# Optimization experiments

Measured on AMD Instinct MI355X. Metric: run time of the kernel, lower is better.

Reference implementation:

```python
import jax, jax.numpy as jnp
import numpy as np

# Geometry / discretization constants (mirrors WaveCell.__init__)
NX, NY = 192, 192
DT = 1e-3
CMAX = 1.0
H = DT * CMAX * np.sqrt(2.0) * 1.01  # auto-set h as in __init__ (satisfies CFL)
SRC_X, SRC_Y = 96, 32  # point source grid location


def _laplacian(y, inv_h2):
    # y: [B, Nx, Ny]; 5-point stencil with zero padding (conv2d padding=1)
    p = jnp.pad(y, ((0, 0), (1, 1), (1, 1)))
    return inv_h2 * (p[:, :-2, 1:-1] + p[:, 2:, 1:-1]
                     + p[:, 1:-1, :-2] + p[:, 1:-1, 2:] - 4.0 * y)


def setup_inputs() -> dict:
    key = jax.random.key(0)
    k1, k2, k3 = jax.random.split(key, 3)
    B, T = 4, 256
    x = jax.random.normal(k1, (B, T, 1), dtype=jnp.float32)
    # per-cell wave speed in [0,1) so cmax <= 1 (CFL-safe)
    c = jax.random.uniform(k2, (NX, NY), dtype=jnp.float32)
    # boundary absorber damping coefficient
    b = jax.random.uniform(k3, (NX, NY), dtype=jnp.float32)
    return {"x": x, "c": c, "b": b}


def reference(x, c, b):
    B, T = x.shape[0], x.shape[1]
    inv_h2 = 1.0 / (H * H)
    inv_dt2 = 1.0 / (DT * DT)
    a_inv = 1.0 / (inv_dt2 + 0.5 * b / DT)   # [Nx, Ny]
    coef2 = inv_dt2 - 0.5 * b / DT           # [Nx, Ny]
    c2 = c * c

    x_seq = jnp.transpose(x[..., 0], (1, 0))  # [T, B]

    def step(carry, xt):
        y1, y2 = carry  # fields one and two steps ago
        y = a_inv * (2.0 * inv_dt2 * y1 - coef2 * y2 + c2 * _laplacian(y1, inv_h2))
        y = y.at[:, SRC_X, SRC_Y].add(xt)  # point source injection
        return (y, y1), y

    y0 = jnp.zeros((B, NX, NY), dtype=x.dtype)
    _, ys = jax.lax.scan(step, (y0, y0), x_seq)  # ys: [T, B, Nx, Ny]
    return jnp.transpose(ys, (1, 0, 2, 3))       # [B, T, Nx, Ny]
```

## Files before the change

kernel.cpp:

```cpp
#include <hip/hip_runtime.h>


#define NXg 192
#define NYg 192
#define BATCH 4
#define TSTEPS 256
#define CELLS (NXg * NYg)

#define TS 24
#define KSTEP 16
#define EXT 56
#define LROWS (EXT + 2)
#define LPITCH 68
#define LSZ (LROWS * LPITCH)
#define NTHREADS 448

#define SRC_X 96
#define SRC_Y 32

__global__ __launch_bounds__(NTHREADS) void wave_tile_kernel(
    const float* __restrict__ cgp, const float* __restrict__ bgp,
    const float* __restrict__ x, float* __restrict__ out, int t0) {
  __shared__ float buf0[LSZ];
  __shared__ float buf1[LSZ];

  const int tid = threadIdx.x;
  const int lr = tid >> 3;
  const int lg = tid & 7;
  const int bcol = blockIdx.x;
  const int brow = blockIdx.y;
  const int bb = blockIdx.z;
  const int r0 = brow * TS - KSTEP;
  const int c0 = bcol * TS - KSTEP;
  const int obase = bb * TSTEPS * CELLS;
  const float inv_h2 = (float)(1.0 / (2.0 * 1.01 * 1.01 * 1.0e-3 * 1.0e-3));

  const int gr = r0 + lr;
  const int gc = c0 + 8 * lg;
  const bool id = (lg < 7) && (gr >= 0) && (gr < NXg) && (gc >= 0) && (gc < NYg);
  const bool til = (lr >= KSTEP) && (lr < KSTEP + TS) && (lg >= 2) && (lg < 5);
  const bool hs = (SRC_X >= r0) && (SRC_X < r0 + EXT) &&
                  (SRC_Y >= c0) && (SRC_Y < c0 + EXT);
  const int gofs = id ? (gr * NYg + gc) : 0;

  const float4 z4 = make_float4(0.f, 0.f, 0.f, 0.f);

  float4 cv0 = z4, cv1 = z4, bv0 = z4, bv1 = z4;
  float4 yc0 = z4, yc1 = z4, yp0 = z4, yp1 = z4;
  if (id) {
    cv0 = *(const float4*)(cgp + gofs);
    cv1 = *(const float4*)(cgp + gofs + 4);
    bv0 = *(const float4*)(bgp + gofs);
    bv1 = *(const float4*)(bgp + gofs + 4);
    if (t0 > 0) {
      yc0 = *(const float4*)(out + obase + (t0 - 1) * CELLS + gofs);
      yc1 = *(const float4*)(out + obase + (t0 - 1) * CELLS + gofs + 4);
      yp0 = *(const float4*)(out + obase + (t0 - 2) * CELLS + gofs);
      yp1 = *(const float4*)(out + obase + (t0 - 2) * CELLS + gofs + 4);
    }
  }
  float xs[KSTEP];
  {
    const float4* xp = (const float4*)(x + bb * TSTEPS + t0);
    float4 a0 = xp[0], a1 = xp[1], a2 = xp[2], a3 = xp[3];
    xs[0] = a0.x; xs[1] = a0.y; xs[2] = a0.z; xs[3] = a0.w;
    xs[4] = a1.x; xs[5] = a1.y; xs[6] = a1.z; xs[7] = a1.w;
    xs[8] = a2.x; xs[9] = a2.y; xs[10] = a2.z; xs[11] = a2.w;
    xs[12] = a3.x; xs[13] = a3.y; xs[14] = a3.z; xs[15] = a3.w;
  }

  float4 Dc0 = z4, Dc1 = z4, Ey0 = z4, Ey1 = z4, G0 = z4, G1 = z4;
  float4 sm0 = z4, sm1 = z4;
  if (id) {
    float ai;
    ai = 1.0f / (1.0e6f + 500.0f * bv0.x);
    Dc0.x = 2.0e6f * ai; Ey0.x = (1.0e6f - 500.0f * bv0.x) * ai;
    G0.x = (cv0.x * cv0.x) * inv_h2 * ai;
    ai = 1.0f / (1.0e6f + 500.0f * bv0.y);
    Dc0.y = 2.0e6f * ai; Ey0.y = (1.0e6f - 500.0f * bv0.y) * ai;
    G0.y = (cv0.y * cv0.y) * inv_h2 * ai;
    ai = 1.0f / (1.0e6f + 500.0f * bv0.z);
    Dc0.z = 2.0e6f * ai; Ey0.z = (1.0e6f - 500.0f * bv0.z) * ai;
    G0.z = (cv0.z * cv0.z) * inv_h2 * ai;
    ai = 1.0f / (1.0e6f + 500.0f * bv0.w);
    Dc0.w = 2.0e6f * ai; Ey0.w = (1.0e6f - 500.0f * bv0.w) * ai;
    G0.w = (cv0.w * cv0.w) * inv_h2 * ai;
    ai = 1.0f / (1.0e6f + 500.0f * bv1.x);
    Dc1.x = 2.0e6f * ai; Ey1.x = (1.0e6f - 500.0f * bv1.x) * ai;
    G1.x = (cv1.x * cv1.x) * inv_h2 * ai;
    ai = 1.0f / (1.0e6f + 500.0f * bv1.y);
    Dc1.y = 2.0e6f * ai; Ey1.y = (1.0e6f - 500.0f * bv1.y) * ai;
    G1.y = (cv1.y * cv1.y) * inv_h2 * ai;
    ai = 1.0f / (1.0e6f + 500.0f * bv1.z);
    Dc1.z = 2.0e6f * ai; Ey1.z = (1.0e6f - 500.0f * bv1.z) * ai;
    G1.z = (cv1.z * cv1.z) * inv_h2 * ai;
    ai = 1.0f / (1.0e6f + 500.0f * bv1.w);
    Dc1.w = 2.0e6f * ai; Ey1.w = (1.0e6f - 500.0f * bv1.w) * ai;
    G1.w = (cv1.w * cv1.w) * inv_h2 * ai;
    if (gr == SRC_X) {
      sm0.x = (gc + 0 == SRC_Y) ? 1.0f : 0.0f;
      sm0.y = (gc + 1 == SRC_Y) ? 1.0f : 0.0f;
      sm0.z = (gc + 2 == SRC_Y) ? 1.0f : 0.0f;
      sm0.w = (gc + 3 == SRC_Y) ? 1.0f : 0.0f;
      sm1.x = (gc + 4 == SRC_Y) ? 1.0f : 0.0f;
      sm1.y = (gc + 5 == SRC_Y) ? 1.0f : 0.0f;
      sm1.z = (gc + 6 == SRC_Y) ? 1.0f : 0.0f;
      sm1.w = (gc + 7 == SRC_Y) ? 1.0f : 0.0f;
    }
  }

  const int lo = (lr + 1) * LPITCH + 4 + 8 * lg;
  *(float4*)&buf0[lo] = yc0;
  *(float4*)&buf0[lo + 4] = yc1;
  __syncthreads();

  float* ping = buf0;
  float* pong = buf1;

  float4 pv0 = z4, pv1 = z4;
  float* pop = out;

#define CELL(dst, up_, dn_, lf_, rt_, D_, E_, Gc_, y_, p_)              \
  {                                                                     \
    float s_ = fmaf(-4.0f, y_, (up_ + dn_) + (lf_ + rt_));              \
    dst = fmaf(Gc_, s_, fmaf(-E_, p_, D_ * y_));                        \
  }

#pragma unroll
  for (int j = 0; j < KSTEP; ++j) {
    const float xt = xs[j];
    float* op = out + obase + (t0 + j) * CELLS;

    if (j > 0 && til) {
      *(float4*)(pop + gofs) = pv0;
      *(float4*)(pop + gofs + 4) = pv1;
    }

    const bool alive = (lr >= j + 1) && (lr <= 54 - j);
    if (alive) {
      float lqw = __shfl_up(yc1.w, 1);
      lqw = (lg == 0) ? 0.0f : lqw;
      float rqx = __shfl_down(yc0.x, 1);
      rqx = (lg == 7) ? 0.0f : rqx;

      float4 up0 = *(float4*)&ping[lo - LPITCH];
      float4 up1 = *(float4*)&ping[lo - LPITCH + 4];
      float4 dn0 = *(float4*)&ping[lo + LPITCH];
      float4 dn1 = *(float4*)&ping[lo + LPITCH + 4];

      float4 val0, val1;
      CELL(val0.x, up0.x, dn0.x, lqw,    yc0.y, Dc0.x, Ey0.x, G0.x, yc0.x, yp0.x);
      CELL(val0.y, up0.y, dn0.y, yc0.x,  yc0.z, Dc0.y, Ey0.y, G0.y, yc0.y, yp0.y);
      CELL(val0.z, up0.z, dn0.z, yc0.y,  yc0.w, Dc0.z, Ey0.z, G0.z, yc0.z, yp0.z);
      CELL(val0.w, up0.w, dn0.w, yc0.z,  yc1.x, Dc0.w, Ey0.w, G0.w, yc0.w, yp0.w);
      CELL(val1.x, up1.x, dn1.x, yc0.w,  yc1.y, Dc1.x, Ey1.x, G1.x, yc1.x, yp1.x);
      CELL(val1.y, up1.y, dn1.y, yc1.x,  yc1.z, Dc1.y, Ey1.y, G1.y, yc1.y, yp1.y);
      CELL(val1.z, up1.z, dn1.z, yc1.y,  yc1.w, Dc1.z, Ey1.z, G1.z, yc1.z, yp1.z);
      CELL(val1.w, up1.w, dn1.w, yc1.z,  rqx,   Dc1.w, Ey1.w, G1.w, yc1.w, yp1.w);

      if (hs) {
        val0.x = fmaf(sm0.x, xt, val0.x);
        val0.y = fmaf(sm0.y, xt, val0.y);
        val0.z = fmaf(sm0.z, xt, val0.z);
        val0.w = fmaf(sm0.w, xt, val0.w);
        val1.x = fmaf(sm1.x, xt, val1.x);
        val1.y = fmaf(sm1.y, xt, val1.y);
        val1.z = fmaf(sm1.z, xt, val1.z);
        val1.w = fmaf(sm1.w, xt, val1.w);
      }

      yp0 = yc0; yp1 = yc1;
      yc0 = val0; yc1 = val1;

      if (j < KSTEP - 1) {
        *(float4*)&pong[lo] = val0;
        *(float4*)&pong[lo + 4] = val1;
      }

      pv0 = val0; pv1 = val1;
    }
    pop = op;

    if (j < KSTEP - 1) {
      asm volatile("s_waitcnt lgkmcnt(0)\n\ts_barrier" ::: "memory");
    }
    float* tmp = ping; ping = pong; pong = tmp;
  }
#undef CELL

  if (til) {
    *(float4*)(pop + gofs) = pv0;
    *(float4*)(pop + gofs + 4) = pv1;
  }
}

extern "C" void kernel_launch(void* const* d_in, const int* in_sizes, int n_in,
                              void* d_out, int out_size, void* d_ws,
                              size_t ws_size, hipStream_t stream) {
  const float* x = (const float*)d_in[0];
  const float* c = (const float*)d_in[1];
  const float* b = (const float*)d_in[2];
  float* out = (float*)d_out;

  dim3 grid(NXg / TS, NYg / TS, BATCH);
  for (int t0 = 0; t0 < TSTEPS; t0 += KSTEP) {
    wave_tile_kernel<<<grid, NTHREADS, 0, stream>>>(c, b, x, out, t0);
  }
}
```

Baseline: 317.9 us.

## Replace per-chunk kernel launches with one cooperative persistent kernel using grid sync

The host loop of 16 kernel launches is replaced by a single cooperative launch. Each block loops over the time chunks and calls a grid-wide sync between them. The per-block coefficients (damping and wave-speed terms) are computed once instead of once per launch. This removes launch gaps and the repeated coefficient setup, in exchange for grid barrier cost, with a fallback to multi-launch if the cooperative launch fails.

```diff
diff --git a/kernel.cpp b/kernel.cpp
--- a/kernel.cpp
+++ b/kernel.cpp
@@ -1,4 +1,7 @@
 #include <hip/hip_runtime.h>
+#include <hip/hip_cooperative_groups.h>
+
+namespace cg = cooperative_groups;
 
 
 #define NXg 192
@@ -18,11 +21,13 @@
 #define SRC_X 96
 #define SRC_Y 32
 
-__global__ __launch_bounds__(NTHREADS) void wave_tile_kernel(
+__global__ __launch_bounds__(NTHREADS) void wave_kernel(
     const float* __restrict__ cgp, const float* __restrict__ bgp,
-    const float* __restrict__ x, float* __restrict__ out, int t0) {
+    const float* __restrict__ x, float* __restrict__ out,
+    int t0b, int t0e) {
   __shared__ float buf0[LSZ];
   __shared__ float buf1[LSZ];
+  cg::grid_group grid = cg::this_grid();
 
   const int tid = threadIdx.x;
   const int lr = tid >> 3;
@@ -45,33 +50,13 @@
 
   const float4 z4 = make_float4(0.f, 0.f, 0.f, 0.f);
 
-  float4 cv0 = z4, cv1 = z4, bv0 = z4, bv1 = z4;
-  float4 yc0 = z4, yc1 = z4, yp0 = z4, yp1 = z4;
-  if (id) {
-    cv0 = *(const float4*)(cgp + gofs);
-    cv1 = *(const float4*)(cgp + gofs + 4);
-    bv0 = *(const float4*)(bgp + gofs);
-    bv1 = *(const float4*)(bgp + gofs + 4);
-    if (t0 > 0) {
-      yc0 = *(const float4*)(out + obase + (t0 - 1) * CELLS + gofs);
-      yc1 = *(const float4*)(out + obase + (t0 - 1) * CELLS + gofs + 4);
-      yp0 = *(const float4*)(out + obase + (t0 - 2) * CELLS + gofs);
-      yp1 = *(const float4*)(out + obase + (t0 - 2) * CELLS + gofs + 4);
-    }
-  }
-  float xs[KSTEP];
-  {
-    const float4* xp = (const float4*)(x + bb * TSTEPS + t0);
-    float4 a0 = xp[0], a1 = xp[1], a2 = xp[2], a3 = xp[3];
-    xs[0] = a0.x; xs[1] = a0.y; xs[2] = a0.z; xs[3] = a0.w;
-    xs[4] = a1.x; xs[5] = a1.y; xs[6] = a1.z; xs[7] = a1.w;
-    xs[8] = a2.x; xs[9] = a2.y; xs[10] = a2.z; xs[11] = a2.w;
-    xs[12] = a3.x; xs[13] = a3.y; xs[14] = a3.z; xs[15] = a3.w;
-  }
-
   float4 Dc0 = z4, Dc1 = z4, Ey0 = z4, Ey1 = z4, G0 = z4, G1 = z4;
   float4 sm0 = z4, sm1 = z4;
   if (id) {
+    float4 cv0 = *(const float4*)(cgp + gofs);
+    float4 cv1 = *(const float4*)(cgp + gofs + 4);
+    float4 bv0 = *(const float4*)(bgp + gofs);
+    float4 bv1 = *(const float4*)(bgp + gofs + 4);
     float ai;
     ai = 1.0f / (1.0e6f + 500.0f * bv0.x);
     Dc0.x = 2.0e6f * ai; Ey0.x = (1.0e6f - 500.0f * bv0.x) * ai;
@@ -110,15 +95,6 @@
   }
 
   const int lo = (lr + 1) * LPITCH + 4 + 8 * lg;
-  *(float4*)&buf0[lo] = yc0;
-  *(float4*)&buf0[lo + 4] = yc1;
-  __syncthreads();
-
-  float* ping = buf0;
-  float* pong = buf1;
-
-  float4 pv0 = z4, pv1 = z4;
-  float* pop = out;
 
 #define CELL(dst, up_, dn_, lf_, rt_, D_, E_, Gc_, y_, p_)              \
   {                                                                     \
@@ -126,72 +102,105 @@
     dst = fmaf(Gc_, s_, fmaf(-E_, p_, D_ * y_));                        \
   }
 
+  for (int t0 = t0b; t0 < t0e; t0 += KSTEP) {
+    if (t0 > t0b) {
+      grid.sync();
+    }
+
+    float4 yc0 = z4, yc1 = z4, yp0 = z4, yp1 = z4;
+    if (id && t0 > 0) {
+      yc0 = *(const float4*)(out + obase + (t0 - 1) * CELLS + gofs);
+      yc1 = *(const float4*)(out + obase + (t0 - 1) * CELLS + gofs + 4);
+      yp0 = *(const float4*)(out + obase + (t0 - 2) * CELLS + gofs);
+      yp1 = *(const float4*)(out + obase + (t0 - 2) * CELLS + gofs + 4);
+    }
+    float xs[KSTEP];
+    {
+      const float4* xp = (const float4*)(x + bb * TSTEPS + t0);
+      float4 a0 = xp[0], a1 = xp[1], a2 = xp[2], a3 = xp[3];
+      xs[0] = a0.x; xs[1] = a0.y; xs[2] = a0.z; xs[3] = a0.w;
+      xs[4] = a1.x; xs[5] = a1.y; xs[6] = a1.z; xs[7] = a1.w;
+      xs[8] = a2.x; xs[9] = a2.y; xs[10] = a2.z; xs[11] = a2.w;
+      xs[12] = a3.x; xs[13] = a3.y; xs[14] = a3.z; xs[15] = a3.w;
+    }
+
+    *(float4*)&buf0[lo] = yc0;
+    *(float4*)&buf0[lo + 4] = yc1;
+    asm volatile("s_waitcnt lgkmcnt(0)\n\ts_barrier" ::: "memory");
+
+    float* ping = buf0;
+    float* pong = buf1;
+
+    float4 pv0 = z4, pv1 = z4;
+    float* pop = out;
+
 #pragma unroll
-  for (int j = 0; j < KSTEP; ++j) {
-    const float xt = xs[j];
-    float* op = out + obase + (t0 + j) * CELLS;
-
-    if (j > 0 && til) {
+    for (int j = 0; j < KSTEP; ++j) {
+      const float xt = xs[j];
+      float* op = out + obase + (t0 + j) * CELLS;
+
+      if (j > 0 && til) {
+        *(float4*)(pop + gofs) = pv0;
+        *(float4*)(pop + gofs + 4) = pv1;
+      }
+
+      const bool alive = (lr >= j + 1) && (lr <= 54 - j);
+      if (alive) {
+        float lqw = __shfl_up(yc1.w, 1);
+        lqw = (lg == 0) ? 0.0f : lqw;
+        float rqx = __shfl_down(yc0.x, 1);
+        rqx = (lg == 7) ? 0.0f : rqx;
+
+        float4 up0 = *(float4*)&ping[lo - LPITCH];
+        float4 up1 = *(float4*)&ping[lo - LPITCH + 4];
+        float4 dn0 = *(float4*)&ping[lo + LPITCH];
+        float4 dn1 = *(float4*)&ping[lo + LPITCH + 4];
+
+        float4 val0, val1;
+        CELL(val0.x, up0.x, dn0.x, lqw,    yc0.y, Dc0.x, Ey0.x, G0.x, yc0.x, yp0.x);
+        CELL(val0.y, up0.y, dn0.y, yc0.x,  yc0.z, Dc0.y, Ey0.y, G0.y, yc0.y, yp0.y);
+        CELL(val0.z, up0.z, dn0.z, yc0.y,  yc0.w, Dc0.z, Ey0.z, G0.z, yc0.z, yp0.z);
+        CELL(val0.w, up0.w, dn0.w, yc0.z,  yc1.x, Dc0.w, Ey0.w, G0.w, yc0.w, yp0.w);
+        CELL(val1.x, up1.x, dn1.x, yc0.w,  yc1.y, Dc1.x, Ey1.x, G1.x, yc1.x, yp1.x);
+        CELL(val1.y, up1.y, dn1.y, yc1.x,  yc1.z, Dc1.y, Ey1.y, G1.y, yc1.y, yp1.y);
+        CELL(val1.z, up1.z, dn1.z, yc1.y,  yc1.w, Dc1.z, Ey1.z, G1.z, yc1.z, yp1.z);
+        CELL(val1.w, up1.w, dn1.w, yc1.z,  rqx,   Dc1.w, Ey1.w, G1.w, yc1.w, yp1.w);
+
+        if (hs) {
+          val0.x = fmaf(sm0.x, xt, val0.x);
+          val0.y = fmaf(sm0.y, xt, val0.y);
+          val0.z = fmaf(sm0.z, xt, val0.z);
+          val0.w = fmaf(sm0.w, xt, val0.w);
+          val1.x = fmaf(sm1.x, xt, val1.x);
+          val1.y = fmaf(sm1.y, xt, val1.y);
+          val1.z = fmaf(sm1.z, xt, val1.z);
+          val1.w = fmaf(sm1.w, xt, val1.w);
+        }
+
+        yp0 = yc0; yp1 = yc1;
+        yc0 = val0; yc1 = val1;
+
+        if (j < KSTEP - 1) {
+          *(float4*)&pong[lo] = val0;
+          *(float4*)&pong[lo + 4] = val1;
+        }
+
+        pv0 = val0; pv1 = val1;
+      }
+      pop = op;
+
+      if (j < KSTEP - 1) {
+        asm volatile("s_waitcnt lgkmcnt(0)\n\ts_barrier" ::: "memory");
+      }
+      float* tmp = ping; ping = pong; pong = tmp;
+    }
+
+    if (til) {
       *(float4*)(pop + gofs) = pv0;
       *(float4*)(pop + gofs + 4) = pv1;
     }
-
-    const bool alive = (lr >= j + 1) && (lr <= 54 - j);
-    if (alive) {
-      float lqw = __shfl_up(yc1.w, 1);
-      lqw = (lg == 0) ? 0.0f : lqw;
-      float rqx = __shfl_down(yc0.x, 1);
-      rqx = (lg == 7) ? 0.0f : rqx;
-
-      float4 up0 = *(float4*)&ping[lo - LPITCH];
-      float4 up1 = *(float4*)&ping[lo - LPITCH + 4];
-      float4 dn0 = *(float4*)&ping[lo + LPITCH];
-      float4 dn1 = *(float4*)&ping[lo + LPITCH + 4];
-
-      float4 val0, val1;
-      CELL(val0.x, up0.x, dn0.x, lqw,    yc0.y, Dc0.x, Ey0.x, G0.x, yc0.x, yp0.x);
-      CELL(val0.y, up0.y, dn0.y, yc0.x,  yc0.z, Dc0.y, Ey0.y, G0.y, yc0.y, yp0.y);
-      CELL(val0.z, up0.z, dn0.z, yc0.y,  yc0.w, Dc0.z, Ey0.z, G0.z, yc0.z, yp0.z);
-      CELL(val0.w, up0.w, dn0.w, yc0.z,  yc1.x, Dc0.w, Ey0.w, G0.w, yc0.w, yp0.w);
-      CELL(val1.x, up1.x, dn1.x, yc0.w,  yc1.y, Dc1.x, Ey1.x, G1.x, yc1.x, yp1.x);
-      CELL(val1.y, up1.y, dn1.y, yc1.x,  yc1.z, Dc1.y, Ey1.y, G1.y, yc1.y, yp1.y);
-      CELL(val1.z, up1.z, dn1.z, yc1.y,  yc1.w, Dc1.z, Ey1.z, G1.z, yc1.z, yp1.z);
-      CELL(val1.w, up1.w, dn1.w, yc1.z,  rqx,   Dc1.w, Ey1.w, G1.w, yc1.w, yp1.w);
-
-      if (hs) {
-        val0.x = fmaf(sm0.x, xt, val0.x);
-        val0.y = fmaf(sm0.y, xt, val0.y);
-        val0.z = fmaf(sm0.z, xt, val0.z);
-        val0.w = fmaf(sm0.w, xt, val0.w);
-        val1.x = fmaf(sm1.x, xt, val1.x);
-        val1.y = fmaf(sm1.y, xt, val1.y);
-        val1.z = fmaf(sm1.z, xt, val1.z);
-        val1.w = fmaf(sm1.w, xt, val1.w);
-      }
-
-      yp0 = yc0; yp1 = yc1;
-      yc0 = val0; yc1 = val1;
-
-      if (j < KSTEP - 1) {
-        *(float4*)&pong[lo] = val0;
-        *(float4*)&pong[lo + 4] = val1;
-      }
-
-      pv0 = val0; pv1 = val1;
-    }
-    pop = op;
-
-    if (j < KSTEP - 1) {
-      asm volatile("s_waitcnt lgkmcnt(0)\n\ts_barrier" ::: "memory");
-    }
-    float* tmp = ping; ping = pong; pong = tmp;
   }
 #undef CELL
-
-  if (til) {
-    *(float4*)(pop + gofs) = pv0;
-    *(float4*)(pop + gofs + 4) = pv1;
-  }
 }
 
 extern "C" void kernel_launch(void* const* d_in, const int* in_sizes, int n_in,
@@ -203,7 +212,15 @@
   float* out = (float*)d_out;
 
   dim3 grid(NXg / TS, NYg / TS, BATCH);
-  for (int t0 = 0; t0 < TSTEPS; t0 += KSTEP) {
-    wave_tile_kernel<<<grid, NTHREADS, 0, stream>>>(c, b, x, out, t0);
+  int t0b = 0, t0e = TSTEPS;
+  const float* ca = c; const float* ba = b; const float* xa = x; float* oa = out;
+  void* args[] = {(void*)&ca, (void*)&ba, (void*)&xa, (void*)&oa,
+                  (void*)&t0b, (void*)&t0e};
+  hipError_t err = hipLaunchCooperativeKernel(
+      (const void*)wave_kernel, grid, dim3(NTHREADS), args, 0, stream);
+  if (err != hipSuccess) {
+    for (int t0 = 0; t0 < TSTEPS; t0 += KSTEP) {
+      wave_kernel<<<grid, NTHREADS, 0, stream>>>(c, b, x, out, t0, t0 + KSTEP);
+    }
   }
 }
```

New measurement: 774.9 us. +143.7%, slower.

## Advance two time steps per barrier using redundant neighbor-row computation

Applied to the files above, without the earlier changes.

Each thread now also computes the rows directly above and below its own at step t, keeping their previous values and coefficients in registers. With those it can produce its row at step t+1 without an LDS round trip, so the number of LDS exchanges and barriers per 16-step launch is halved. The cost is about three times the stencil arithmetic per step, more registers for the extra coefficients and history, and extra zeroed halo rows in shared memory.

```diff
diff --git a/kernel.cpp b/kernel.cpp
--- a/kernel.cpp
+++ b/kernel.cpp
@@ -10,7 +10,7 @@
 #define TS 24
 #define KSTEP 16
 #define EXT 56
-#define LROWS (EXT + 2)
+#define LROWS 60
 #define LPITCH 68
 #define LSZ (LROWS * LPITCH)
 #define NTHREADS 448
@@ -18,7 +18,42 @@
 #define SRC_X 96
 #define SRC_Y 32
 
-__global__ __launch_bounds__(NTHREADS) void wave_tile_kernel(
+__device__ __forceinline__ void mkcoef(float4 cv, float4 bv, float inv_h2,
+                                       float4& D, float4& E, float4& Gq) {
+  float ai;
+  ai = 1.0f / (1.0e6f + 500.0f * bv.x);
+  D.x = 2.0e6f * ai; E.x = (1.0e6f - 500.0f * bv.x) * ai; Gq.x = cv.x * cv.x * inv_h2 * ai;
+  ai = 1.0f / (1.0e6f + 500.0f * bv.y);
+  D.y = 2.0e6f * ai; E.y = (1.0e6f - 500.0f * bv.y) * ai; Gq.y = cv.y * cv.y * inv_h2 * ai;
+  ai = 1.0f / (1.0e6f + 500.0f * bv.z);
+  D.z = 2.0e6f * ai; E.z = (1.0e6f - 500.0f * bv.z) * ai; Gq.z = cv.z * cv.z * inv_h2 * ai;
+  ai = 1.0f / (1.0e6f + 500.0f * bv.w);
+  D.w = 2.0e6f * ai; E.w = (1.0e6f - 500.0f * bv.w) * ai; Gq.w = cv.w * cv.w * inv_h2 * ai;
+}
+
+#define CELL(dst, up_, dn_, lf_, rt_, D_, E_, G_, y_, p_)             \
+  {                                                                   \
+    float s_ = fmaf(-4.0f, y_, (up_ + dn_) + (lf_ + rt_));            \
+    dst = fmaf(G_, s_, fmaf(-E_, p_, D_ * y_));                       \
+  }
+
+#define ROW8(vA, vB, uA, uB, dA, dB, cA, cB, lq, rq, Da, Db, Ea, Eb, Ga, Gb, pA, pB) \
+  CELL(vA.x, uA.x, dA.x, lq,   cA.y, Da.x, Ea.x, Ga.x, cA.x, pA.x);   \
+  CELL(vA.y, uA.y, dA.y, cA.x, cA.z, Da.y, Ea.y, Ga.y, cA.y, pA.y);   \
+  CELL(vA.z, uA.z, dA.z, cA.y, cA.w, Da.z, Ea.z, Ga.z, cA.z, pA.z);   \
+  CELL(vA.w, uA.w, dA.w, cA.z, cB.x, Da.w, Ea.w, Ga.w, cA.w, pA.w);   \
+  CELL(vB.x, uB.x, dB.x, cA.w, cB.y, Db.x, Eb.x, Gb.x, cB.x, pB.x);   \
+  CELL(vB.y, uB.y, dB.y, cB.x, cB.z, Db.y, Eb.y, Gb.y, cB.y, pB.y);   \
+  CELL(vB.z, uB.z, dB.z, cB.y, cB.w, Db.z, Eb.z, Gb.z, cB.z, pB.z);   \
+  CELL(vB.w, uB.w, dB.w, cB.z, rq,   Db.w, Eb.w, Gb.w, cB.w, pB.w);
+
+#define ADDSRC(vA, vB, sA, sB, xt_)                                   \
+  vA.x = fmaf(sA.x, xt_, vA.x); vA.y = fmaf(sA.y, xt_, vA.y);         \
+  vA.z = fmaf(sA.z, xt_, vA.z); vA.w = fmaf(sA.w, xt_, vA.w);         \
+  vB.x = fmaf(sB.x, xt_, vB.x); vB.y = fmaf(sB.y, xt_, vB.y);         \
+  vB.z = fmaf(sB.z, xt_, vB.z); vB.w = fmaf(sB.w, xt_, vB.w);
+
+__global__ __launch_bounds__(NTHREADS) void wave_kernel(
     const float* __restrict__ cgp, const float* __restrict__ bgp,
     const float* __restrict__ x, float* __restrict__ out, int t0) {
   __shared__ float buf0[LSZ];
@@ -37,26 +72,75 @@
 
   const int gr = r0 + lr;
   const int gc = c0 + 8 * lg;
-  const bool id = (lg < 7) && (gr >= 0) && (gr < NXg) && (gc >= 0) && (gc < NYg);
+  const bool colOK = (lg < 7) && (gc >= 0) && (gc < NYg);
+  const bool idC = colOK && (gr >= 0) && (gr < NXg);
+  const bool idU = colOK && (gr - 1 >= 0) && (gr - 1 < NXg);
+  const bool idD = colOK && (gr + 1 >= 0) && (gr + 1 < NXg);
   const bool til = (lr >= KSTEP) && (lr < KSTEP + TS) && (lg >= 2) && (lg < 5);
-  const bool hs = (SRC_X >= r0) && (SRC_X < r0 + EXT) &&
+  const bool hs = (SRC_X >= r0 - 1) && (SRC_X <= r0 + EXT) &&
                   (SRC_Y >= c0) && (SRC_Y < c0 + EXT);
-  const int gofs = id ? (gr * NYg + gc) : 0;
+  const int ofsC = idC ? (gr * NYg + gc) : 0;
+  const int ofsU = idU ? ((gr - 1) * NYg + gc) : 0;
+  const int ofsD = idD ? ((gr + 1) * NYg + gc) : 0;
 
   const float4 z4 = make_float4(0.f, 0.f, 0.f, 0.f);
 
-  float4 cv0 = z4, cv1 = z4, bv0 = z4, bv1 = z4;
-  float4 yc0 = z4, yc1 = z4, yp0 = z4, yp1 = z4;
-  if (id) {
-    cv0 = *(const float4*)(cgp + gofs);
-    cv1 = *(const float4*)(cgp + gofs + 4);
-    bv0 = *(const float4*)(bgp + gofs);
-    bv1 = *(const float4*)(bgp + gofs + 4);
-    if (t0 > 0) {
-      yc0 = *(const float4*)(out + obase + (t0 - 1) * CELLS + gofs);
-      yc1 = *(const float4*)(out + obase + (t0 - 1) * CELLS + gofs + 4);
-      yp0 = *(const float4*)(out + obase + (t0 - 2) * CELLS + gofs);
-      yp1 = *(const float4*)(out + obase + (t0 - 2) * CELLS + gofs + 4);
+  float4 Dc0 = z4, Dc1 = z4, Ey0 = z4, Ey1 = z4, G0 = z4, G1 = z4;
+  float4 DU0 = z4, DU1 = z4, EU0 = z4, EU1 = z4, GU0 = z4, GU1 = z4;
+  float4 DD0 = z4, DD1 = z4, ED0 = z4, ED1 = z4, GD0 = z4, GD1 = z4;
+  if (idC) {
+    mkcoef(*(const float4*)(cgp + ofsC), *(const float4*)(bgp + ofsC), inv_h2, Dc0, Ey0, G0);
+    mkcoef(*(const float4*)(cgp + ofsC + 4), *(const float4*)(bgp + ofsC + 4), inv_h2, Dc1, Ey1, G1);
+  }
+  if (idU) {
+    mkcoef(*(const float4*)(cgp + ofsU), *(const float4*)(bgp + ofsU), inv_h2, DU0, EU0, GU0);
+    mkcoef(*(const float4*)(cgp + ofsU + 4), *(const float4*)(bgp + ofsU + 4), inv_h2, DU1, EU1, GU1);
+  }
+  if (idD) {
+    mkcoef(*(const float4*)(cgp + ofsD), *(const float4*)(bgp + ofsD), inv_h2, DD0, ED0, GD0);
+    mkcoef(*(const float4*)(cgp + ofsD + 4), *(const float4*)(bgp + ofsD + 4), inv_h2, DD1, ED1, GD1);
+  }
+
+  float4 smc0 = z4, smc1 = z4;
+  if (colOK) {
+    smc0.x = (gc + 0 == SRC_Y) ? 1.0f : 0.0f;
+    smc0.y = (gc + 1 == SRC_Y) ? 1.0f : 0.0f;
+    smc0.z = (gc + 2 == SRC_Y) ? 1.0f : 0.0f;
+    smc0.w = (gc + 3 == SRC_Y) ? 1.0f : 0.0f;
+    smc1.x = (gc + 4 == SRC_Y) ? 1.0f : 0.0f;
+    smc1.y = (gc + 5 == SRC_Y) ? 1.0f : 0.0f;
+    smc1.z = (gc + 6 == SRC_Y) ? 1.0f : 0.0f;
+    smc1.w = (gc + 7 == SRC_Y) ? 1.0f : 0.0f;
+  }
+  const float fU = (gr - 1 == SRC_X) ? 1.0f : 0.0f;
+  const float fC = (gr == SRC_X) ? 1.0f : 0.0f;
+  const float fD = (gr + 1 == SRC_X) ? 1.0f : 0.0f;
+  float4 smU0, smU1, smC0, smC1, smD0, smD1;
+  smU0.x = smc0.x * fU; smU0.y = smc0.y * fU; smU0.z = smc0.z * fU; smU0.w = smc0.w * fU;
+  smU1.x = smc1.x * fU; smU1.y = smc1.y * fU; smU1.z = smc1.z * fU; smU1.w = smc1.w * fU;
+  smC0.x = smc0.x * fC; smC0.y = smc0.y * fC; smC0.z = smc0.z * fC; smC0.w = smc0.w * fC;
+  smC1.x = smc1.x * fC; smC1.y = smc1.y * fC; smC1.z = smc1.z * fC; smC1.w = smc1.w * fC;
+  smD0.x = smc0.x * fD; smD0.y = smc0.y * fD; smD0.z = smc0.z * fD; smD0.w = smc0.w * fD;
+  smD1.x = smc1.x * fD; smD1.y = smc1.y * fD; smD1.z = smc1.z * fD; smD1.w = smc1.w * fD;
+
+  float4 yc0 = z4, yc1 = z4;
+  float4 ypc0 = z4, ypc1 = z4, ypu0 = z4, ypu1 = z4, ypd0 = z4, ypd1 = z4;
+  if (t0 > 0) {
+    const float* o1 = out + obase + (t0 - 1) * CELLS;
+    const float* o2 = out + obase + (t0 - 2) * CELLS;
+    if (idC) {
+      yc0 = *(const float4*)(o1 + ofsC);
+      yc1 = *(const float4*)(o1 + ofsC + 4);
+      ypc0 = *(const float4*)(o2 + ofsC);
+      ypc1 = *(const float4*)(o2 + ofsC + 4);
+    }
+    if (idU) {
+      ypu0 = *(const float4*)(o2 + ofsU);
+      ypu1 = *(const float4*)(o2 + ofsU + 4);
+    }
+    if (idD) {
+      ypd0 = *(const float4*)(o2 + ofsD);
+      ypd1 = *(const float4*)(o2 + ofsD + 4);
     }
   }
   float xs[KSTEP];
@@ -69,128 +153,88 @@
     xs[12] = a3.x; xs[13] = a3.y; xs[14] = a3.z; xs[15] = a3.w;
   }
 
-  float4 Dc0 = z4, Dc1 = z4, Ey0 = z4, Ey1 = z4, G0 = z4, G1 = z4;
-  float4 sm0 = z4, sm1 = z4;
-  if (id) {
-    float ai;
-    ai = 1.0f / (1.0e6f + 500.0f * bv0.x);
-    Dc0.x = 2.0e6f * ai; Ey0.x = (1.0e6f - 500.0f * bv0.x) * ai;
-    G0.x = (cv0.x * cv0.x) * inv_h2 * ai;
-    ai = 1.0f / (1.0e6f + 500.0f * bv0.y);
-    Dc0.y = 2.0e6f * ai; Ey0.y = (1.0e6f - 500.0f * bv0.y) * ai;
-    G0.y = (cv0.y * cv0.y) * inv_h2 * ai;
-    ai = 1.0f / (1.0e6f + 500.0f * bv0.z);
-    Dc0.z = 2.0e6f * ai; Ey0.z = (1.0e6f - 500.0f * bv0.z) * ai;
-    G0.z = (cv0.z * cv0.z) * inv_h2 * ai;
-    ai = 1.0f / (1.0e6f + 500.0f * bv0.w);
-    Dc0.w = 2.0e6f * ai; Ey0.w = (1.0e6f - 500.0f * bv0.w) * ai;
-    G0.w = (cv0.w * cv0.w) * inv_h2 * ai;
-    ai = 1.0f / (1.0e6f + 500.0f * bv1.x);
-    Dc1.x = 2.0e6f * ai; Ey1.x = (1.0e6f - 500.0f * bv1.x) * ai;
-    G1.x = (cv1.x * cv1.x) * inv_h2 * ai;
-    ai = 1.0f / (1.0e6f + 500.0f * bv1.y);
-    Dc1.y = 2.0e6f * ai; Ey1.y = (1.0e6f - 500.0f * bv1.y) * ai;
-    G1.y = (cv1.y * cv1.y) * inv_h2 * ai;
-    ai = 1.0f / (1.0e6f + 500.0f * bv1.z);
-    Dc1.z = 2.0e6f * ai; Ey1.z = (1.0e6f - 500.0f * bv1.z) * ai;
-    G1.z = (cv1.z * cv1.z) * inv_h2 * ai;
-    ai = 1.0f / (1.0e6f + 500.0f * bv1.w);
-    Dc1.w = 2.0e6f * ai; Ey1.w = (1.0e6f - 500.0f * bv1.w) * ai;
-    G1.w = (cv1.w * cv1.w) * inv_h2 * ai;
-    if (gr == SRC_X) {
-      sm0.x = (gc + 0 == SRC_Y) ? 1.0f : 0.0f;
-      sm0.y = (gc + 1 == SRC_Y) ? 1.0f : 0.0f;
-      sm0.z = (gc + 2 == SRC_Y) ? 1.0f : 0.0f;
-      sm0.w = (gc + 3 == SRC_Y) ? 1.0f : 0.0f;
-      sm1.x = (gc + 4 == SRC_Y) ? 1.0f : 0.0f;
-      sm1.y = (gc + 5 == SRC_Y) ? 1.0f : 0.0f;
-      sm1.z = (gc + 6 == SRC_Y) ? 1.0f : 0.0f;
-      sm1.w = (gc + 7 == SRC_Y) ? 1.0f : 0.0f;
-    }
-  }
-
-  const int lo = (lr + 1) * LPITCH + 4 + 8 * lg;
+  const int lo = (lr + 2) * LPITCH + 4 + 8 * lg;
+
+  if (tid < 136) {
+    float* bufp = (tid < 68) ? buf0 : buf1;
+    const int q2 = tid % 68;
+    const int grow = q2 / 17;
+    const int row = (grow < 2) ? grow : (56 + grow);
+    *(float4*)&bufp[row * LPITCH + 4 * (q2 % 17)] = z4;
+  }
+
   *(float4*)&buf0[lo] = yc0;
   *(float4*)&buf0[lo + 4] = yc1;
-  __syncthreads();
+  asm volatile("s_waitcnt lgkmcnt(0)\n\ts_barrier" ::: "memory");
 
   float* ping = buf0;
   float* pong = buf1;
 
-  float4 pv0 = z4, pv1 = z4;
-  float* pop = out;
-
-#define CELL(dst, up_, dn_, lf_, rt_, D_, E_, Gc_, y_, p_)              \
-  {                                                                     \
-    float s_ = fmaf(-4.0f, y_, (up_ + dn_) + (lf_ + rt_));              \
-    dst = fmaf(Gc_, s_, fmaf(-E_, p_, D_ * y_));                        \
-  }
-
 #pragma unroll
-  for (int j = 0; j < KSTEP; ++j) {
-    const float xt = xs[j];
-    float* op = out + obase + (t0 + j) * CELLS;
-
-    if (j > 0 && til) {
-      *(float4*)(pop + gofs) = pv0;
-      *(float4*)(pop + gofs + 4) = pv1;
-    }
-
-    const bool alive = (lr >= j + 1) && (lr <= 54 - j);
-    if (alive) {
-      float lqw = __shfl_up(yc1.w, 1);
-      lqw = (lg == 0) ? 0.0f : lqw;
-      float rqx = __shfl_down(yc0.x, 1);
-      rqx = (lg == 7) ? 0.0f : rqx;
-
-      float4 up0 = *(float4*)&ping[lo - LPITCH];
-      float4 up1 = *(float4*)&ping[lo - LPITCH + 4];
-      float4 dn0 = *(float4*)&ping[lo + LPITCH];
-      float4 dn1 = *(float4*)&ping[lo + LPITCH + 4];
-
-      float4 val0, val1;
-      CELL(val0.x, up0.x, dn0.x, lqw,    yc0.y, Dc0.x, Ey0.x, G0.x, yc0.x, yp0.x);
-      CELL(val0.y, up0.y, dn0.y, yc0.x,  yc0.z, Dc0.y, Ey0.y, G0.y, yc0.y, yp0.y);
-      CELL(val0.z, up0.z, dn0.z, yc0.y,  yc0.w, Dc0.z, Ey0.z, G0.z, yc0.z, yp0.z);
-      CELL(val0.w, up0.w, dn0.w, yc0.z,  yc1.x, Dc0.w, Ey0.w, G0.w, yc0.w, yp0.w);
-      CELL(val1.x, up1.x, dn1.x, yc0.w,  yc1.y, Dc1.x, Ey1.x, G1.x, yc1.x, yp1.x);
-      CELL(val1.y, up1.y, dn1.y, yc1.x,  yc1.z, Dc1.y, Ey1.y, G1.y, yc1.y, yp1.y);
-      CELL(val1.z, up1.z, dn1.z, yc1.y,  yc1.w, Dc1.z, Ey1.z, G1.z, yc1.z, yp1.z);
-      CELL(val1.w, up1.w, dn1.w, yc1.z,  rqx,   Dc1.w, Ey1.w, G1.w, yc1.w, yp1.w);
-
-      if (hs) {
-        val0.x = fmaf(sm0.x, xt, val0.x);
-        val0.y = fmaf(sm0.y, xt, val0.y);
-        val0.z = fmaf(sm0.z, xt, val0.z);
-        val0.w = fmaf(sm0.w, xt, val0.w);
-        val1.x = fmaf(sm1.x, xt, val1.x);
-        val1.y = fmaf(sm1.y, xt, val1.y);
-        val1.z = fmaf(sm1.z, xt, val1.z);
-        val1.w = fmaf(sm1.w, xt, val1.w);
-      }
-
-      yp0 = yc0; yp1 = yc1;
-      yc0 = val0; yc1 = val1;
-
-      if (j < KSTEP - 1) {
-        *(float4*)&pong[lo] = val0;
-        *(float4*)&pong[lo + 4] = val1;
-      }
-
-      pv0 = val0; pv1 = val1;
-    }
-    pop = op;
-
-    if (j < KSTEP - 1) {
+  for (int k = 0; k < KSTEP / 2; ++k) {
+    const float xtA = xs[2 * k];
+    const float xtB = xs[2 * k + 1];
+
+    float4 u20 = *(float4*)&ping[lo - 2 * LPITCH];
+    float4 u21 = *(float4*)&ping[lo - 2 * LPITCH + 4];
+    float4 u10 = *(float4*)&ping[lo - LPITCH];
+    float4 u11 = *(float4*)&ping[lo - LPITCH + 4];
+    float4 d10 = *(float4*)&ping[lo + LPITCH];
+    float4 d11 = *(float4*)&ping[lo + LPITCH + 4];
+    float4 d20 = *(float4*)&ping[lo + 2 * LPITCH];
+    float4 d21 = *(float4*)&ping[lo + 2 * LPITCH + 4];
+
+    float lqU = __shfl_up(u11.w, 1);   lqU = (lg == 0) ? 0.0f : lqU;
+    float rqU = __shfl_down(u10.x, 1); rqU = (lg == 7) ? 0.0f : rqU;
+    float lqC = __shfl_up(yc1.w, 1);   lqC = (lg == 0) ? 0.0f : lqC;
+    float rqC = __shfl_down(yc0.x, 1); rqC = (lg == 7) ? 0.0f : rqC;
+    float lqD = __shfl_up(d11.w, 1);   lqD = (lg == 0) ? 0.0f : lqD;
+    float rqD = __shfl_down(d10.x, 1); rqD = (lg == 7) ? 0.0f : rqD;
+
+    float4 vU0, vU1, vC0, vC1, vD0, vD1;
+    ROW8(vU0, vU1, u20, u21, yc0, yc1, u10, u11, lqU, rqU,
+         DU0, DU1, EU0, EU1, GU0, GU1, ypu0, ypu1);
+    ROW8(vC0, vC1, u10, u11, d10, d11, yc0, yc1, lqC, rqC,
+         Dc0, Dc1, Ey0, Ey1, G0, G1, ypc0, ypc1);
+    ROW8(vD0, vD1, yc0, yc1, d20, d21, d10, d11, lqD, rqD,
+         DD0, DD1, ED0, ED1, GD0, GD1, ypd0, ypd1);
+    if (hs) {
+      ADDSRC(vU0, vU1, smU0, smU1, xtA);
+      ADDSRC(vC0, vC1, smC0, smC1, xtA);
+      ADDSRC(vD0, vD1, smD0, smD1, xtA);
+    }
+
+    float lqB = __shfl_up(vC1.w, 1);   lqB = (lg == 0) ? 0.0f : lqB;
+    float rqB = __shfl_down(vC0.x, 1); rqB = (lg == 7) ? 0.0f : rqB;
+    float4 w0, w1;
+    ROW8(w0, w1, vU0, vU1, vD0, vD1, vC0, vC1, lqB, rqB,
+         Dc0, Dc1, Ey0, Ey1, G0, G1, yc0, yc1);
+    if (hs) {
+      ADDSRC(w0, w1, smC0, smC1, xtB);
+    }
+
+    if (til) {
+      float* opA = out + obase + (t0 + 2 * k) * CELLS;
+      *(float4*)(opA + ofsC) = vC0;
+      *(float4*)(opA + ofsC + 4) = vC1;
+      float* opB = opA + CELLS;
+      *(float4*)(opB + ofsC) = w0;
+      *(float4*)(opB + ofsC + 4) = w1;
+    }
+
+    if (k < KSTEP / 2 - 1) {
+      *(float4*)&pong[lo] = w0;
+      *(float4*)&pong[lo + 4] = w1;
+    }
+    ypu0 = vU0; ypu1 = vU1;
+    ypc0 = vC0; ypc1 = vC1;
+    ypd0 = vD0; ypd1 = vD1;
+    yc0 = w0; yc1 = w1;
+
+    if (k < KSTEP / 2 - 1) {
       asm volatile("s_waitcnt lgkmcnt(0)\n\ts_barrier" ::: "memory");
     }
     float* tmp = ping; ping = pong; pong = tmp;
-  }
-#undef CELL
-
-  if (til) {
-    *(float4*)(pop + gofs) = pv0;
-    *(float4*)(pop + gofs + 4) = pv1;
   }
 }
 
@@ -204,6 +248,6 @@
 
   dim3 grid(NXg / TS, NYg / TS, BATCH);
   for (int t0 = 0; t0 < TSTEPS; t0 += KSTEP) {
-    wave_tile_kernel<<<grid, NTHREADS, 0, stream>>>(c, b, x, out, t0);
+    wave_kernel<<<grid, NTHREADS, 0, stream>>>(c, b, x, out, t0);
   }
 }
```

Result: slower. 396.8 us (+24.8%).
